# Kernel optimization log

Measured on AMD Instinct MI355X. Metric: run time of the kernel, lower is better.

## Reference

```python
import jax, jax.numpy as jnp
import numpy as np

B, S, H = 64, 2048, 512


def setup_inputs() -> dict:
    key = jax.random.key(0)
    k1, k2, k3, k4, k5 = jax.random.split(key, 5)
    scale = 1.0 / np.sqrt(H)
    return {
        "decoder_hidden": jax.random.normal(k1, (B, H), dtype=jnp.float32),
        "encoder_outputs": jax.random.normal(k2, (B, S, H), dtype=jnp.float32),
        "W_q": jax.random.normal(k3, (H, H), dtype=jnp.float32) * scale,
        "W_k": jax.random.normal(k4, (H, H), dtype=jnp.float32) * scale,
        "v": jax.random.normal(k5, (H,), dtype=jnp.float32) * scale,
    }


def reference(decoder_hidden, encoder_outputs, W_q, W_k, v):
    # query: [B,H] -> [B,1,H]; torch Linear computes x @ W.T
    query = (decoder_hidden @ W_q.T)[:, None, :]          # [B,1,H]
    keys = jnp.einsum('bsh,gh->bsg', encoder_outputs, W_k)  # [B,S,H]
    energy = jnp.tanh(query + keys)                        # [B,S,H]
    scores = jnp.einsum('bsh,h->bs', energy, v)            # [B,S]
    attention_weights = jax.nn.softmax(scores, axis=1)     # [B,S]
    context = jnp.einsum('bs,bsh->bh', attention_weights, encoder_outputs)
    return context, attention_weights
```

## Files before the change

kernel.cpp:

```cpp
#include <hip/hip_runtime.h>
#include <hip/hip_bf16.h>
#include <cstdint>


typedef __attribute__((ext_vector_type(8))) short short8;
typedef __attribute__((ext_vector_type(4))) float f32x4;

__device__ __forceinline__ unsigned short f2bf(float f) {
    unsigned u = __builtin_bit_cast(unsigned, f);
    u += 0x7FFFu + ((u >> 16) & 1u);
    return (unsigned short)(u >> 16);
}

__device__ __forceinline__ float tanh_fast(float x) {
    float e = __expf(2.0f * x);
    return 1.0f - 2.0f * __builtin_amdgcn_rcpf(e + 1.0f);
}

__device__ __forceinline__ void async16(const unsigned short* g, short* l) {
    __builtin_amdgcn_global_load_lds(
        (const __attribute__((address_space(1))) unsigned int*)g,
        (__attribute__((address_space(3))) unsigned int*)l, 16, 0, 0);
}

__global__ void cast_wk_kernel(const float* __restrict__ wk, unsigned short* __restrict__ wkb,
                               float* __restrict__ numer) {
    int i = (blockIdx.x * 256 + threadIdx.x) * 4;
    float4 f = *(const float4*)(wk + i);
    ushort4 o;
    o.x = f2bf(f.x); o.y = f2bf(f.y); o.z = f2bf(f.z); o.w = f2bf(f.w);
    *(ushort4*)(wkb + i) = o;
    if (blockIdx.x < 32) {
        *(float4*)(numer + i) = (float4){0.f, 0.f, 0.f, 0.f};
    }
}

__global__ void q_kernel(const float* __restrict__ dec, const float* __restrict__ wq,
                         float* __restrict__ q) {
    int b  = blockIdx.x >> 3;
    int g0 = (blockIdx.x & 7) * 64;
    int t = threadIdx.x, lane = t & 63, w = t >> 6;
    __shared__ float dls[512];
    dls[t] = dec[b * 512 + t];
    dls[t + 256] = dec[b * 512 + 256 + t];
    __syncthreads();
    #pragma unroll
    for (int gi = 0; gi < 16; ++gi) {
        int g = g0 + w + gi * 4;
        float acc = 0.f;
        #pragma unroll
        for (int it = 0; it < 2; ++it) {
            int h = (it * 64 + lane) * 4;
            float4 wv = *(const float4*)(wq + (size_t)g * 512 + h);
            acc += wv.x * dls[h] + wv.y * dls[h + 1] + wv.z * dls[h + 2] + wv.w * dls[h + 3];
        }
        #pragma unroll
        for (int m = 32; m; m >>= 1) acc += __shfl_xor(acc, m, 64);
        if (lane == 0) q[b * 512 + g] = acc;
    }
}

__launch_bounds__(256, 2)
__global__ void scores_kernel(const float* __restrict__ enc, const unsigned short* __restrict__ wkb,
                              const float* __restrict__ q, const float* __restrict__ v,
                              float* __restrict__ scores, float* __restrict__ numer) {
    __shared__ __align__(16) short Bs[2][512 * 32];
    __shared__ __align__(16) short As[2][64 * 40];
    __shared__ float q_s[512];
    __shared__ float v_s[512];
    __shared__ float red[4][64];
    __shared__ float w_lds[64];

    int t = threadIdx.x, lane = t & 63, w = t >> 6;
    int quad = lane >> 4, l15 = lane & 15;
    int tile = blockIdx.x;
    int b = tile >> 5;
    size_t m0 = (size_t)tile * 64;

    q_s[t] = q[b * 512 + t];   q_s[t + 256] = q[b * 512 + 256 + t];
    v_s[t] = v[t];             v_s[t + 256] = v[t + 256];

    f32x4 acc[4][8];
    #pragma unroll
    for (int i = 0; i < 4; ++i)
        #pragma unroll
        for (int j = 0; j < 8; ++j)
            acc[i][j] = (f32x4){0.f, 0.f, 0.f, 0.f};

    int arow = t >> 2, akq = t & 3;
    const float* aptr = enc + (m0 + arow) * 512 + akq * 8;

    int kqs = (lane & 3) ^ ((lane >> 3) & 3);
    const unsigned short* bgbase = wkb + (size_t)(w * 16 + (lane >> 2)) * 512 + kqs * 8;
    int blo = (w * 16 + (lane >> 2)) * 32 + (lane & 3) * 8;
    short* blbase0 = &Bs[0][blo];
    short* blbase1 = &Bs[1][blo];

    float4 nfa0 = *(const float4*)(aptr);
    float4 nfa1 = *(const float4*)(aptr + 4);
    #pragma unroll
    for (int i = 0; i < 8; ++i)
        async16(bgbase + (size_t)i * 64 * 512, blbase0 + i * 64 * 32);
    {
        short8 av;
        av[0] = (short)f2bf(nfa0.x); av[1] = (short)f2bf(nfa0.y);
        av[2] = (short)f2bf(nfa0.z); av[3] = (short)f2bf(nfa0.w);
        av[4] = (short)f2bf(nfa1.x); av[5] = (short)f2bf(nfa1.y);
        av[6] = (short)f2bf(nfa1.z); av[7] = (short)f2bf(nfa1.w);
        *(short8*)&As[0][arow * 40 + akq * 8] = av;
    }
    __syncthreads();

    #pragma unroll
    for (int ks = 0; ks < 16; ++ks) {
        const int cur = ks & 1, nxt = cur ^ 1;
        const int kk = ks * 32;
        if (ks < 15) {
            nfa0 = *(const float4*)(aptr + kk + 32);
            nfa1 = *(const float4*)(aptr + kk + 36);
            short* bl = nxt ? blbase1 : blbase0;
            #pragma unroll
            for (int i = 0; i < 8; ++i)
                async16(bgbase + (size_t)i * 64 * 512 + kk + 32, bl + i * 64 * 32);
        }
        short8 af[4];
        #pragma unroll
        for (int mt = 0; mt < 4; ++mt)
            af[mt] = *(short8*)&As[cur][(mt * 16 + l15) * 40 + quad * 8];
        #pragma unroll
        for (int nt = 0; nt < 8; ++nt) {
            int brow = w * 128 + nt * 16 + l15;
            short8 bf = *(short8*)&Bs[cur][brow * 32 + (quad ^ ((l15 >> 1) & 3)) * 8];
            #pragma unroll
            for (int mt = 0; mt < 4; ++mt)
                acc[mt][nt] = __builtin_amdgcn_mfma_f32_16x16x32_bf16(af[mt], bf, acc[mt][nt], 0, 0, 0);
        }
        if (ks < 15) {
            short8 av;
            av[0] = (short)f2bf(nfa0.x); av[1] = (short)f2bf(nfa0.y);
            av[2] = (short)f2bf(nfa0.z); av[3] = (short)f2bf(nfa0.w);
            av[4] = (short)f2bf(nfa1.x); av[5] = (short)f2bf(nfa1.y);
            av[6] = (short)f2bf(nfa1.z); av[7] = (short)f2bf(nfa1.w);
            *(short8*)&As[nxt][arow * 40 + akq * 8] = av;
        }
        __syncthreads();
    }

    float rs[4][4];
    #pragma unroll
    for (int mt = 0; mt < 4; ++mt)
        #pragma unroll
        for (int r = 0; r < 4; ++r) rs[mt][r] = 0.f;
    #pragma unroll
    for (int nt = 0; nt < 8; ++nt) {
        int g = w * 128 + nt * 16 + l15;
        float qb = q_s[g], vv = v_s[g];
        #pragma unroll
        for (int mt = 0; mt < 4; ++mt)
            #pragma unroll
            for (int r = 0; r < 4; ++r)
                rs[mt][r] += tanh_fast(qb + acc[mt][nt][r]) * vv;
    }
    #pragma unroll
    for (int m = 1; m <= 8; m <<= 1)
        #pragma unroll
        for (int mt = 0; mt < 4; ++mt)
            #pragma unroll
            for (int r = 0; r < 4; ++r)
                rs[mt][r] += __shfl_xor(rs[mt][r], m, 64);
    if (l15 == 0) {
        #pragma unroll
        for (int mt = 0; mt < 4; ++mt)
            #pragma unroll
            for (int r = 0; r < 4; ++r)
                red[w][mt * 16 + quad * 4 + r] = rs[mt][r];
    }
    __syncthreads();
    if (t < 64) {
        float sc = red[0][t] + red[1][t] + red[2][t] + red[3][t];
        scores[m0 + t] = sc;
        w_lds[t] = __expf(sc);
    }
    __syncthreads();

    {
        float n0 = 0.f, n1 = 0.f;
        const float* ep = enc + m0 * 512 + t * 2;
        #pragma unroll 16
        for (int s = 0; s < 64; ++s) {
            float wv = w_lds[s];
            float2 e = *(const float2*)(ep + (size_t)s * 512);
            n0 += wv * e.x; n1 += wv * e.y;
        }
        float* np = numer + b * 512 + t * 2;
        atomicAdd(np, n0);
        atomicAdd(np + 1, n1);
    }
}

__global__ void softmax_kernel(float* __restrict__ out, const float* __restrict__ numer) {
    int b = blockIdx.x, t = threadIdx.x, lane = t & 63, w = t >> 6;
    float* sc = out + 32768 + b * 2048;
    __shared__ float wred[4];
    float vals[8];
    float mx = -1e30f;
    #pragma unroll
    for (int i = 0; i < 8; ++i) { vals[i] = sc[t + i * 256]; mx = fmaxf(mx, vals[i]); }
    #pragma unroll
    for (int m = 32; m; m >>= 1) mx = fmaxf(mx, __shfl_xor(mx, m, 64));
    if (lane == 0) wred[w] = mx;
    __syncthreads();
    mx = fmaxf(fmaxf(wred[0], wred[1]), fmaxf(wred[2], wred[3]));
    __syncthreads();
    float s = 0.f;
    #pragma unroll
    for (int i = 0; i < 8; ++i) { vals[i] = __expf(vals[i] - mx); s += vals[i]; }
    #pragma unroll
    for (int m = 32; m; m >>= 1) s += __shfl_xor(s, m, 64);
    if (lane == 0) wred[w] = s;
    __syncthreads();
    s = wred[0] + wred[1] + wred[2] + wred[3];
    float inv = 1.0f / s;
    #pragma unroll
    for (int i = 0; i < 8; ++i) sc[t + i * 256] = vals[i] * inv;
    float csc = __expf(-mx) * inv;
    out[b * 512 + t]       = numer[b * 512 + t] * csc;
    out[b * 512 + 256 + t] = numer[b * 512 + 256 + t] * csc;
}

extern "C" void kernel_launch(void* const* d_in, const int* in_sizes, int n_in,
                              void* d_out, int out_size, void* d_ws, size_t ws_size,
                              hipStream_t stream) {
    const float* dec = (const float*)d_in[0];
    const float* enc = (const float*)d_in[1];
    const float* wq  = (const float*)d_in[2];
    const float* wk  = (const float*)d_in[3];
    const float* v   = (const float*)d_in[4];
    float* out = (float*)d_out;

    unsigned short* wkb = (unsigned short*)d_ws;
    float* q = (float*)((char*)d_ws + 512 * 512 * 2);
    float* numer = (float*)((char*)d_ws + 512 * 512 * 2 + 64 * 512 * 4);

    cast_wk_kernel<<<256, 256, 0, stream>>>(wk, wkb, numer);
    q_kernel<<<512, 256, 0, stream>>>(dec, wq, q);
    scores_kernel<<<2048, 256, 0, stream>>>(enc, wkb, q, v, out + 32768, numer);
    softmax_kernel<<<64, 256, 0, stream>>>(out, numer);
}
```

Before: 447.3 us.

## Double scores-kernel M tile to 128 rows with 8 waves sharing each W_k tile

The scores kernel now processes 128 encoder rows per block with 512 threads (8 waves as a 2x4 grid), so each bf16 W_k k-slice loaded into LDS is reused by twice as many rows. This halves total W_k traffic and the number of numerator atomics per batch. The context reduction switches to one column per thread with four independent accumulators. The cost is fewer blocks (1024) and a larger per-block footprint, which may reduce occupancy and latency hiding.

Measured after the change: 462.8 us. 1.03x slower.

```diff
diff --git a/kernel.cpp b/kernel.cpp
--- a/kernel.cpp
+++ b/kernel.cpp
@@ -10,6 +10,15 @@
     unsigned u = __builtin_bit_cast(unsigned, f);
     u += 0x7FFFu + ((u >> 16) & 1u);
     return (unsigned short)(u >> 16);
+}
+
+__device__ __forceinline__ short8 cvt8(float4 a, float4 b) {
+    short8 r;
+    r[0] = (short)f2bf(a.x); r[1] = (short)f2bf(a.y);
+    r[2] = (short)f2bf(a.z); r[3] = (short)f2bf(a.w);
+    r[4] = (short)f2bf(b.x); r[5] = (short)f2bf(b.y);
+    r[6] = (short)f2bf(b.z); r[7] = (short)f2bf(b.w);
+    return r;
 }
 
 __device__ __forceinline__ float tanh_fast(float x) {
@@ -60,25 +69,26 @@
     }
 }
 
-__launch_bounds__(256, 2)
+__launch_bounds__(512)
 __global__ void scores_kernel(const float* __restrict__ enc, const unsigned short* __restrict__ wkb,
                               const float* __restrict__ q, const float* __restrict__ v,
                               float* __restrict__ scores, float* __restrict__ numer) {
     __shared__ __align__(16) short Bs[2][512 * 32];
-    __shared__ __align__(16) short As[2][64 * 40];
+    __shared__ __align__(16) short As[2][128][40];
     __shared__ float q_s[512];
     __shared__ float v_s[512];
-    __shared__ float red[4][64];
-    __shared__ float w_lds[64];
+    __shared__ float red[4][128];
+    __shared__ float w_lds[128];
 
     int t = threadIdx.x, lane = t & 63, w = t >> 6;
+    int wr = w >> 2, wc = w & 3;
     int quad = lane >> 4, l15 = lane & 15;
     int tile = blockIdx.x;
-    int b = tile >> 5;
-    size_t m0 = (size_t)tile * 64;
-
-    q_s[t] = q[b * 512 + t];   q_s[t + 256] = q[b * 512 + 256 + t];
-    v_s[t] = v[t];             v_s[t + 256] = v[t + 256];
+    int b = tile >> 4;
+    size_t m0 = (size_t)tile * 128;
+
+    q_s[t] = q[b * 512 + t];
+    v_s[t] = v[t];
 
     f32x4 acc[4][8];
     #pragma unroll
@@ -93,21 +103,14 @@
     int kqs = (lane & 3) ^ ((lane >> 3) & 3);
     const unsigned short* bgbase = wkb + (size_t)(w * 16 + (lane >> 2)) * 512 + kqs * 8;
     int blo = (w * 16 + (lane >> 2)) * 32 + (lane & 3) * 8;
-    short* blbase0 = &Bs[0][blo];
-    short* blbase1 = &Bs[1][blo];
-
-    float4 nfa0 = *(const float4*)(aptr);
-    float4 nfa1 = *(const float4*)(aptr + 4);
-    #pragma unroll
-    for (int i = 0; i < 8; ++i)
-        async16(bgbase + (size_t)i * 64 * 512, blbase0 + i * 64 * 32);
+
     {
-        short8 av;
-        av[0] = (short)f2bf(nfa0.x); av[1] = (short)f2bf(nfa0.y);
-        av[2] = (short)f2bf(nfa0.z); av[3] = (short)f2bf(nfa0.w);
-        av[4] = (short)f2bf(nfa1.x); av[5] = (short)f2bf(nfa1.y);
-        av[6] = (short)f2bf(nfa1.z); av[7] = (short)f2bf(nfa1.w);
-        *(short8*)&As[0][arow * 40 + akq * 8] = av;
+        float4 fa0 = *(const float4*)(aptr);
+        float4 fa1 = *(const float4*)(aptr + 4);
+        #pragma unroll
+        for (int i = 0; i < 4; ++i)
+            async16(bgbase + (size_t)i * 128 * 512, &Bs[0][blo + i * 128 * 32]);
+        *(short8*)&As[0][arow][akq * 8] = cvt8(fa0, fa1);
     }
     __syncthreads();
 
@@ -115,34 +118,28 @@
     for (int ks = 0; ks < 16; ++ks) {
         const int cur = ks & 1, nxt = cur ^ 1;
         const int kk = ks * 32;
+        float4 nfa0, nfa1;
         if (ks < 15) {
             nfa0 = *(const float4*)(aptr + kk + 32);
             nfa1 = *(const float4*)(aptr + kk + 36);
-            short* bl = nxt ? blbase1 : blbase0;
-            #pragma unroll
-            for (int i = 0; i < 8; ++i)
-                async16(bgbase + (size_t)i * 64 * 512 + kk + 32, bl + i * 64 * 32);
+            #pragma unroll
+            for (int i = 0; i < 4; ++i)
+                async16(bgbase + (size_t)i * 128 * 512 + kk + 32, &Bs[nxt][blo + i * 128 * 32]);
         }
         short8 af[4];
         #pragma unroll
         for (int mt = 0; mt < 4; ++mt)
-            af[mt] = *(short8*)&As[cur][(mt * 16 + l15) * 40 + quad * 8];
+            af[mt] = *(short8*)&As[cur][wr * 64 + mt * 16 + l15][quad * 8];
         #pragma unroll
         for (int nt = 0; nt < 8; ++nt) {
-            int brow = w * 128 + nt * 16 + l15;
+            int brow = wc * 128 + nt * 16 + l15;
             short8 bf = *(short8*)&Bs[cur][brow * 32 + (quad ^ ((l15 >> 1) & 3)) * 8];
             #pragma unroll
             for (int mt = 0; mt < 4; ++mt)
                 acc[mt][nt] = __builtin_amdgcn_mfma_f32_16x16x32_bf16(af[mt], bf, acc[mt][nt], 0, 0, 0);
         }
-        if (ks < 15) {
-            short8 av;
-            av[0] = (short)f2bf(nfa0.x); av[1] = (short)f2bf(nfa0.y);
-            av[2] = (short)f2bf(nfa0.z); av[3] = (short)f2bf(nfa0.w);
-            av[4] = (short)f2bf(nfa1.x); av[5] = (short)f2bf(nfa1.y);
-            av[6] = (short)f2bf(nfa1.z); av[7] = (short)f2bf(nfa1.w);
-            *(short8*)&As[nxt][arow * 40 + akq * 8] = av;
-        }
+        if (ks < 15)
+            *(short8*)&As[nxt][arow][akq * 8] = cvt8(nfa0, nfa1);
         __syncthreads();
     }
 
@@ -153,7 +150,7 @@
         for (int r = 0; r < 4; ++r) rs[mt][r] = 0.f;
     #pragma unroll
     for (int nt = 0; nt < 8; ++nt) {
-        int g = w * 128 + nt * 16 + l15;
+        int g = wc * 128 + nt * 16 + l15;
         float qb = q_s[g], vv = v_s[g];
         #pragma unroll
         for (int mt = 0; mt < 4; ++mt)
@@ -173,10 +170,10 @@
         for (int mt = 0; mt < 4; ++mt)
             #pragma unroll
             for (int r = 0; r < 4; ++r)
-                red[w][mt * 16 + quad * 4 + r] = rs[mt][r];
-    }
-    __syncthreads();
-    if (t < 64) {
+                red[wc][wr * 64 + mt * 16 + quad * 4 + r] = rs[mt][r];
+    }
+    __syncthreads();
+    if (t < 128) {
         float sc = red[0][t] + red[1][t] + red[2][t] + red[3][t];
         scores[m0 + t] = sc;
         w_lds[t] = __expf(sc);
@@ -184,17 +181,16 @@
     __syncthreads();
 
     {
-        float n0 = 0.f, n1 = 0.f;
-        const float* ep = enc + m0 * 512 + t * 2;
-        #pragma unroll 16
-        for (int s = 0; s < 64; ++s) {
-            float wv = w_lds[s];
-            float2 e = *(const float2*)(ep + (size_t)s * 512);
-            n0 += wv * e.x; n1 += wv * e.y;
-        }
-        float* np = numer + b * 512 + t * 2;
-        atomicAdd(np, n0);
-        atomicAdd(np + 1, n1);
+        float n0 = 0.f, n1 = 0.f, n2 = 0.f, n3 = 0.f;
+        const float* ep = enc + m0 * 512 + t;
+        #pragma unroll 8
+        for (int s = 0; s < 128; s += 4) {
+            n0 += w_lds[s]     * ep[(size_t)(s)     * 512];
+            n1 += w_lds[s + 1] * ep[(size_t)(s + 1) * 512];
+            n2 += w_lds[s + 2] * ep[(size_t)(s + 2) * 512];
+            n3 += w_lds[s + 3] * ep[(size_t)(s + 3) * 512];
+        }
+        atomicAdd(numer + b * 512 + t, (n0 + n1) + (n2 + n3));
     }
 }
 
@@ -244,6 +240,6 @@
 
     cast_wk_kernel<<<256, 256, 0, stream>>>(wk, wkb, numer);
     q_kernel<<<512, 256, 0, stream>>>(dec, wq, q);
-    scores_kernel<<<2048, 256, 0, stream>>>(enc, wkb, q, v, out + 32768, numer);
+    scores_kernel<<<1024, 512, 0, stream>>>(enc, wkb, q, v, out + 32768, numer);
     softmax_kernel<<<64, 256, 0, stream>>>(out, numer);
 }
```
